# Kernel tuning notes

Measured on AMD Instinct MI355X. Metric: run time of the kernel, lower is better.

The kernel has to match this reference:

```python
import jax, jax.numpy as jnp
import numpy as np

B, L, H, NL = 32, 1024, 4, 2
D_BERT, D_PHY, D_ACC = 1024, 7, 2
C_IN = D_BERT + D_PHY + D_ACC
D = 32
K = 20
N = B * L
E = N * K


def setup_inputs() -> dict:
    key = jax.random.key(0)
    ks = jax.random.split(key, 10)
    return {
        "protbert": jax.random.normal(ks[0], (B, 1, L, D_BERT), jnp.float32),
        "phychem": jax.random.normal(ks[1], (B, 1, L, D_PHY), jnp.float32),
        "resacc": jax.random.normal(ks[2], (B, 1, L, D_ACC), jnp.float32),
        "edge_feat": jax.random.normal(ks[3], (E, 2), jnp.float32),
        "src_idx": jax.random.randint(ks[4], (E,), 0, N, jnp.int32),
        "dst_idx": (jnp.arange(E, dtype=jnp.int32) % N),  # every node gets exactly K in-edges
        "conv_w": jax.random.normal(ks[5], (D, C_IN, 7), jnp.float32) * 0.02,
        "conv_b": jnp.zeros((D,), jnp.float32),
        "bn_gamma": jnp.ones((D,), jnp.float32),
        "bn_beta": jnp.zeros((D,), jnp.float32),
        "bn_mean": jnp.zeros((D,), jnp.float32),
        "bn_var": jnp.ones((D,), jnp.float32),
        "fc_w": jax.random.normal(ks[6], (NL, H, D, D), jnp.float32) * 0.1,
        "attn_w": jax.random.normal(ks[7], (NL, H, 2 * D + 2), jnp.float32) * 0.1,
        "fc_edge_w": jax.random.normal(ks[8], (NL, H, D, 2), jnp.float32) * 0.1,
        "fc_eatt_w": jax.random.normal(ks[9], (NL, H, 2, 2), jnp.float32) * 0.1,
    }


def _leaky(x):
    return jnp.where(x >= 0, x, 0.01 * x)


def _seg_softmax(e, dst, n):
    # softmax over incoming edges of each destination node (DGL mailbox softmax)
    m = jax.ops.segment_max(e, dst, num_segments=n)
    ex = jnp.exp(e - m[dst])
    s = jax.ops.segment_sum(ex, dst, num_segments=n)
    return ex / s[dst]


def reference(protbert, phychem, resacc, edge_feat, src_idx, dst_idx,
              conv_w, conv_b, bn_gamma, bn_beta, bn_mean, bn_var,
              fc_w, attn_w, fc_edge_w, fc_eatt_w):
    # --- Conv1d + LeakyReLU + BatchNorm1d (eval) encoder ---
    x = jnp.concatenate([protbert, phychem, resacc], axis=3)[:, 0]  # (B,L,C_IN)
    x = jnp.transpose(x, (0, 2, 1))  # (B,C_IN,L)
    x = jax.lax.conv_general_dilated(x, conv_w, (1,), [(3, 3)],
                                     dimension_numbers=("NCH", "OIH", "NCH"))
    x = _leaky(x + conv_b[None, :, None])
    scale = (bn_gamma / jnp.sqrt(bn_var + 1e-5))[None, :, None]
    x = (x - bn_mean[None, :, None]) * scale + bn_beta[None, :, None]
    feats = jnp.transpose(x, (0, 2, 1))  # (B,L,D)

    # --- stacked multi-head EGRET layers on flattened batched graph ---
    h = feats.reshape(N, D)
    alpha = None
    for l in range(NL):
        z = jnp.einsum("nd,hod->nho", h, fc_w[l])                    # (N,H,D)
        ex_t = jnp.einsum("ef,hgf->ehg", edge_feat, fc_eatt_w[l])    # (E,H,2) transformed edge feats for attn
        ez = jnp.einsum("ef,hof->eho", edge_feat, fc_edge_w[l])      # (E,H,D) edge messages
        a_src = attn_w[l][:, :D]
        a_dst = attn_w[l][:, D:2 * D]
        a_e = attn_w[l][:, 2 * D:]
        s_src = jnp.einsum("nhd,hd->nh", z, a_src)                   # node-level partial scores
        s_dst = jnp.einsum("nhd,hd->nh", z, a_dst)
        e = _leaky(s_src[src_idx] + s_dst[dst_idx]
                   + jnp.einsum("ehg,hg->eh", ex_t, a_e))            # (E,H)
        alpha = _seg_softmax(e, dst_idx, N)                          # (E,H)
        msg = alpha[:, :, None] * (z[src_idx] + ez)                  # attn on node+edge messages
        h = jax.ops.segment_sum(msg, dst_idx, num_segments=N).mean(axis=1)  # merge='avg'

    feats2 = h.reshape(B, L, D)
    out = jnp.concatenate([feats2, feats], axis=2)  # (B,L,2D)
    return out, alpha
```

## Files before the change

kernel.cpp:

```cpp
#include <hip/hip_runtime.h>
#include <hip/hip_bf16.h>
#include <cstdint>

#define B_   32
#define L_   1024
#define H_   4
#define NL_  2
#define D_   32
#define K_   20
#define N_   (B_ * L_)
#define E_   (N_ * K_)

typedef __attribute__((ext_vector_type(8))) __bf16 bf16x8;
typedef __attribute__((ext_vector_type(4))) float  f32x4;
typedef __attribute__((ext_vector_type(2))) float  f32x2;
typedef __attribute__((ext_vector_type(4))) int    i32x4;

static __device__ __forceinline__ float leaky1(float x) { return x >= 0.f ? x : 0.01f * x; }

static __device__ __forceinline__ bf16x8 cvt8(f32x4 lo, f32x4 hi) {
    bf16x8 r;
    r[0] = (__bf16)lo[0]; r[1] = (__bf16)lo[1]; r[2] = (__bf16)lo[2]; r[3] = (__bf16)lo[3];
    r[4] = (__bf16)hi[0]; r[5] = (__bf16)hi[1]; r[6] = (__bf16)hi[2]; r[7] = (__bf16)hi[3];
    return r;
}

#define GLD_LDS16(g, l) __builtin_amdgcn_global_load_lds( \
    (const __attribute__((address_space(1))) void*)(g),   \
    (__attribute__((address_space(3))) void*)(l), 16, 0, 0)

__global__ __launch_bounds__(256) void k_prep_wb(const float* __restrict__ conv_w,
                                                 __bf16* __restrict__ wb) {
    int idx = blockIdx.x * 256 + threadIdx.x;
    if (idx >= 7 * 32 * 1024) return;
    int t = idx >> 15;
    int r = idx & 32767;
    int d = r >> 10;
    int c = r & 1023;
    wb[idx] = (__bf16)conv_w[d * 7231 + c * 7 + t];
}

#define XR4 262
__global__ __launch_bounds__(256) void k_conv_part(
    const float* __restrict__ protbert, const __bf16* __restrict__ wb,
    float* __restrict__ pbuf) {
    __shared__ __bf16 Xs[2][XR4 * 32];
    __shared__ __bf16 Bs[2][224 * 32];

    const int tid  = threadIdx.x;
    const int tok0 = blockIdx.x * 256;
    const int b    = tok0 >> 10;
    const int lb   = tok0 & 1023;
    const int cb0  = blockIdx.y * 256;

    const float* agp[5];
    int aoffv[5];
    bool ex[5];
    #pragma unroll
    for (int q = 0; q < 5; ++q) {
        int u = (q < 4) ? q * 256 + tid : 1024 + tid;
        bool e = (q < 4) || (tid < 24);
        int row = u >> 2, slot = u & 3;
        int l = lb + row - 3;
        ex[q] = e;
        aoffv[q] = row * 32 + 8 * (slot ^ ((row >> 1) & 3));
        agp[q] = (e && (unsigned)l < 1024u)
            ? protbert + ((size_t)b * 1024 + l) * 1024 + cb0 + slot * 8 : nullptr;
    }

    const int w     = tid >> 6;
    const int lane  = tid & 63;
    const int row16 = lane & 15;
    const int kgrp  = lane >> 4;
    const int d0    = lane & 15;
    const int bslot0 = 8 * (kgrp ^ ((d0 >> 1) & 3));

    const int blrow = lane >> 2;
    const int bsl   = lane & 3;
#define STAGE_B(kc_, bf_) do {                                              \
        for (int c = w; c < 14; c += 4) {                                   \
            int brow_ = c * 16 + blrow;                                     \
            int dd_ = brow_ & 31;                                           \
            int scol_ = 8 * (bsl ^ ((dd_ >> 1) & 3));                       \
            const __bf16* gp_ = wb + (size_t)brow_ * 1024 + cb0 + (kc_) * 32 + scol_; \
            GLD_LDS16(gp_, &Bs[bf_][c * 512]);                              \
        }                                                                   \
    } while (0)

    f32x4 acc[4][2];
    #pragma unroll
    for (int mt = 0; mt < 4; ++mt) {
        acc[mt][0] = (f32x4){0.f, 0.f, 0.f, 0.f};
        acc[mt][1] = (f32x4){0.f, 0.f, 0.f, 0.f};
    }

    {
        f32x4 pl[5], ph[5];
        #pragma unroll
        for (int q = 0; q < 5; ++q) {
            pl[q] = (f32x4){0,0,0,0}; ph[q] = (f32x4){0,0,0,0};
            if (agp[q]) { pl[q] = ((const f32x4*)agp[q])[0]; ph[q] = ((const f32x4*)agp[q])[1]; }
        }
        STAGE_B(0, 0);
        #pragma unroll
        for (int q = 0; q < 5; ++q)
            if (ex[q]) *(bf16x8*)(&Xs[0][aoffv[q]]) = cvt8(pl[q], ph[q]);
    }
    __syncthreads();

    int buf = 0;
    for (int kk = 0; kk < 8; ++kk) {
        f32x4 nl[5], nh[5];
        if (kk < 7) {
            #pragma unroll
            for (int q = 0; q < 5; ++q) {
                nl[q] = (f32x4){0,0,0,0}; nh[q] = (f32x4){0,0,0,0};
                if (agp[q]) {
                    nl[q] = ((const f32x4*)agp[q])[(kk + 1) * 8];
                    nh[q] = ((const f32x4*)agp[q])[(kk + 1) * 8 + 1];
                }
            }
            STAGE_B(kk + 1, buf ^ 1);
        }
        #pragma unroll
        for (int t = 0; t < 7; ++t) {
            bf16x8 b0 = *(const bf16x8*)(&Bs[buf][(t * 32 + d0) * 32 + bslot0]);
            bf16x8 b1 = *(const bf16x8*)(&Bs[buf][(t * 32 + 16 + d0) * 32 + bslot0]);
            #pragma unroll
            for (int mt = 0; mt < 4; ++mt) {
                int arow = w * 64 + mt * 16 + row16 + t;
                bf16x8 a = *(const bf16x8*)(&Xs[buf][arow * 32 + 8 * (kgrp ^ ((arow >> 1) & 3))]);
                acc[mt][0] = __builtin_amdgcn_mfma_f32_16x16x32_bf16(a, b0, acc[mt][0], 0, 0, 0);
                acc[mt][1] = __builtin_amdgcn_mfma_f32_16x16x32_bf16(a, b1, acc[mt][1], 0, 0, 0);
            }
        }
        if (kk < 7) {
            #pragma unroll
            for (int q = 0; q < 5; ++q)
                if (ex[q]) *(bf16x8*)(&Xs[buf ^ 1][aoffv[q]]) = cvt8(nl[q], nh[q]);
        }
        __syncthreads();
        buf ^= 1;
    }

    float* pb = pbuf + ((size_t)blockIdx.y * N_ + tok0) * 32;
    #pragma unroll
    for (int mt = 0; mt < 4; ++mt)
        #pragma unroll
        for (int i = 0; i < 4; ++i) {
            int lrow = w * 64 + mt * 16 + kgrp * 4 + i;
            pb[lrow * 32 + d0]      = acc[mt][0][i];
            pb[lrow * 32 + 16 + d0] = acc[mt][1][i];
        }
}

#define AROWS 70
__global__ __launch_bounds__(256) void k_epi_z0(
    const float* __restrict__ pbuf,     const float* __restrict__ phychem,
    const float* __restrict__ resacc,   const float* __restrict__ conv_w,
    const float* __restrict__ conv_b,   const float* __restrict__ bn_gamma,
    const float* __restrict__ bn_beta,  const float* __restrict__ bn_mean,
    const float* __restrict__ bn_var,   const float* __restrict__ fc_w,
    const float* __restrict__ attn_w,
    float* __restrict__ out, __bf16* __restrict__ z,
    float* __restrict__ ssrc, float* __restrict__ sdst) {
    __shared__ float WT[4 * 1028];
    __shared__ float As[4 * 33], Ad[4 * 33];
    __shared__ float x9[AROWS * 9];
    __shared__ float w9[9 * 7 * 32];
    __shared__ float bnA[32], bnB[32], cb[32];
    __shared__ float fs[64 * 36];

    const int tid  = threadIdx.x;
    const int tok0 = blockIdx.x * 64;
    const int b    = tok0 >> 10;
    const int lb   = tok0 & 1023;

    for (int i = tid; i < 4096; i += 256) {
        int h = i >> 10, rem = i & 1023, o = rem >> 5, d = rem & 31;
        WT[h * 1028 + d * 32 + o] = fc_w[i];
    }
    {
        int h = tid >> 6, o = tid & 63;
        float v = attn_w[h * 66 + o];
        if (o < 32) As[h * 33 + o] = v; else Ad[h * 33 + (o - 32)] = v;
    }
    for (int i = tid; i < 9 * 7 * 32; i += 256) {
        int d = i & 31, jt = i >> 5, t = jt % 7, j = jt / 7;
        w9[i] = conv_w[d * 7231 + (1024 + j) * 7 + t];
    }
    for (int i = tid; i < AROWS * 9; i += 256) {
        int r = i / 9, j = i % 9;
        int l = lb + r - 3;
        float v = 0.f;
        if ((unsigned)l < 1024u)
            v = (j < 7) ? phychem[(b * 1024 + l) * 7 + j] : resacc[(b * 1024 + l) * 2 + (j - 7)];
        x9[i] = v;
    }
    if (tid < 32) {
        float sc = bn_gamma[tid] * rsqrtf(bn_var[tid] + 1e-5f);
        bnA[tid] = sc;
        bnB[tid] = bn_beta[tid] - bn_mean[tid] * sc;
        cb[tid]  = conv_b[tid];
    }
    __syncthreads();

    {
        const int d  = tid & 31;
        const int r0 = tid >> 5;
        #pragma unroll
        for (int q = 0; q < 8; ++q) {
            int lrow = r0 * 8 + q;
            int tok  = tok0 + lrow;
            float s = pbuf[(size_t)tok * 32 + d]
                    + pbuf[(size_t)(N_ + tok) * 32 + d]
                    + pbuf[(size_t)(2 * N_ + tok) * 32 + d]
                    + pbuf[(size_t)(3 * N_ + tok) * 32 + d];
            float c = 0.f;
            #pragma unroll
            for (int t = 0; t < 7; ++t) {
                const float* xr = &x9[(lrow + t) * 9];
                #pragma unroll
                for (int j = 0; j < 9; ++j) c += xr[j] * w9[(j * 7 + t) * 32 + d];
            }
            float v = leaky1(s + c + cb[d]) * bnA[d] + bnB[d];
            out[(size_t)tok * 64 + 32 + d] = v;
            fs[lrow * 36 + d] = v;
        }
    }
    __syncthreads();

    {
        const int nl = tid >> 2;
        const int h  = tid & 3;
        const int n  = tok0 + nl;

        float hrow[32];
        const f32x4* h4 = (const f32x4*)(&fs[nl * 36]);
        #pragma unroll
        for (int q = 0; q < 8; ++q) {
            f32x4 v = h4[q];
            hrow[q * 4 + 0] = v[0]; hrow[q * 4 + 1] = v[1];
            hrow[q * 4 + 2] = v[2]; hrow[q * 4 + 3] = v[3];
        }
        float zz[32];
        #pragma unroll
        for (int o = 0; o < 32; ++o) zz[o] = 0.f;
        #pragma unroll
        for (int d = 0; d < 32; ++d) {
            float hv = hrow[d];
            const f32x4* wt = (const f32x4*)&WT[h * 1028 + d * 32];
            #pragma unroll
            for (int o4 = 0; o4 < 8; ++o4) {
                f32x4 wv = wt[o4];
                zz[o4 * 4 + 0] += hv * wv[0]; zz[o4 * 4 + 1] += hv * wv[1];
                zz[o4 * 4 + 2] += hv * wv[2]; zz[o4 * 4 + 3] += hv * wv[3];
            }
        }
        float s1 = 0.f, s2 = 0.f;
        #pragma unroll
        for (int o = 0; o < 32; ++o) {
            s1 += zz[o] * As[h * 33 + o];
            s2 += zz[o] * Ad[h * 33 + o];
        }
        bf16x8* zo = (bf16x8*)(z + (size_t)n * 128 + h * 32);
        #pragma unroll
        for (int q = 0; q < 4; ++q) {
            bf16x8 v;
            #pragma unroll
            for (int j = 0; j < 8; ++j) v[j] = (__bf16)zz[q * 8 + j];
            zo[q] = v;
        }
        ssrc[n * 4 + h] = s1;
        sdst[n * 4 + h] = s2;
    }
}

__global__ __launch_bounds__(256) void k_z(
    const float* __restrict__ hin, const float* __restrict__ fc_w,
    const float* __restrict__ attn_w, int layer,
    __bf16* __restrict__ z, float* __restrict__ ssrc, float* __restrict__ sdst) {
    __shared__ float WT[4 * 1028];
    __shared__ float As[4 * 33], Ad[4 * 33];

    const int tid = threadIdx.x;
    for (int i = tid; i < 4096; i += 256) {
        int h = i >> 10, rem = i & 1023, o = rem >> 5, d = rem & 31;
        WT[h * 1028 + d * 32 + o] = fc_w[layer * 4096 + i];
    }
    {
        int h = tid >> 6, o = tid & 63;
        float v = attn_w[layer * (4 * 66) + h * 66 + o];
        if (o < 32) As[h * 33 + o] = v; else Ad[h * 33 + (o - 32)] = v;
    }
    __syncthreads();

    const int n = blockIdx.x * 64 + (tid >> 2);
    const int h = tid & 3;

    float hrow[32];
    const f32x4* h4 = (const f32x4*)(hin + (size_t)n * 32);
    #pragma unroll
    for (int q = 0; q < 8; ++q) {
        f32x4 v = h4[q];
        hrow[q * 4 + 0] = v[0]; hrow[q * 4 + 1] = v[1];
        hrow[q * 4 + 2] = v[2]; hrow[q * 4 + 3] = v[3];
    }

    float zz[32];
    #pragma unroll
    for (int o = 0; o < 32; ++o) zz[o] = 0.f;
    #pragma unroll
    for (int d = 0; d < 32; ++d) {
        float hv = hrow[d];
        const f32x4* wt = (const f32x4*)&WT[h * 1028 + d * 32];
        #pragma unroll
        for (int o4 = 0; o4 < 8; ++o4) {
            f32x4 wv = wt[o4];
            zz[o4 * 4 + 0] += hv * wv[0]; zz[o4 * 4 + 1] += hv * wv[1];
            zz[o4 * 4 + 2] += hv * wv[2]; zz[o4 * 4 + 3] += hv * wv[3];
        }
    }
    float s1 = 0.f, s2 = 0.f;
    #pragma unroll
    for (int o = 0; o < 32; ++o) {
        s1 += zz[o] * As[h * 33 + o];
        s2 += zz[o] * Ad[h * 33 + o];
    }
    bf16x8* zo = (bf16x8*)(z + (size_t)n * 128 + h * 32);
    #pragma unroll
    for (int q = 0; q < 4; ++q) {
        bf16x8 v;
        #pragma unroll
        for (int j = 0; j < 8; ++j) v[j] = (__bf16)zz[q * 8 + j];
        zo[q] = v;
    }
    ssrc[n * 4 + h] = s1;
    sdst[n * 4 + h] = s2;
}

__global__ __launch_bounds__(256) void k_node(
    const __bf16* __restrict__ z, const float* __restrict__ ssrc,
    const float* __restrict__ sdst, const int* __restrict__ src_idx,
    const float* __restrict__ edge_feat, const float* __restrict__ attn_w,
    const float* __restrict__ fc_edge_w, const float* __restrict__ fc_eatt_w,
    int layer, float* __restrict__ hout, int hout_stride,
    float* __restrict__ alpha_out) {
    __shared__ float sWe0[4 * 32], sWe1[4 * 32];
    __shared__ float sP[4][2];
    __shared__ float sAl[4][4][24];
    __shared__ float sF[4][4][2];
    __shared__ float sEf[4][20][2];
    __shared__ int   sS[4][24];

    const int tid = threadIdx.x;
    {
        int f = tid & 1, dd = (tid >> 1) & 31, h = tid >> 6;
        float v = fc_edge_w[layer * 256 + tid];
        if (f == 0) sWe0[h * 32 + dd] = v; else sWe1[h * 32 + dd] = v;
        if (tid < 8) {
            int hh = tid >> 1, ff = tid & 1;
            float ae0 = attn_w[layer * 264 + hh * 66 + 64];
            float ae1 = attn_w[layer * 264 + hh * 66 + 65];
            float w0  = fc_eatt_w[layer * 16 + hh * 4 + 0 + ff];
            float w1  = fc_eatt_w[layer * 16 + hh * 4 + 2 + ff];
            sP[hh][ff] = ae0 * w0 + ae1 * w1;
        }
    }
    const int slot = tid >> 6, tn = tid & 63;
    const int n = blockIdx.x * 4 + slot;
    __syncthreads();

    {
        int h = tn & 3;
        float sdv = sdst[n * 4 + h];
        #pragma unroll
        for (int p = 0; p < 2; ++p) {
            int k = p * 16 + (tn >> 2);
            if (p == 0 || tn < 16) {
                int e = n + k * N_;
                int s = src_idx[e];
                f32x2 ef = *(const f32x2*)(edge_feat + (size_t)e * 2);
                float sc = ssrc[s * 4 + h] + sdv + ef.x * sP[h][0] + ef.y * sP[h][1];
                sAl[slot][h][k] = leaky1(sc);
                if (h == 0) { sS[slot][k] = s; sEf[slot][k][0] = ef.x; sEf[slot][k][1] = ef.y; }
            }
        }
    }
    __syncthreads();

    if (tn < 4) {
        int h = tn;
        float m = -1e30f;
        for (int k = 0; k < 20; ++k) m = fmaxf(m, sAl[slot][h][k]);
        float ssum = 0.f;
        for (int k = 0; k < 20; ++k) {
            float v = __expf(sAl[slot][h][k] - m);
            sAl[slot][h][k] = v;
            ssum += v;
        }
        float inv = 1.f / ssum;
        float F0 = 0.f, F1 = 0.f;
        for (int k = 0; k < 20; ++k) {
            float a = sAl[slot][h][k] * inv;
            sAl[slot][h][k] = a;
            F0 += a * sEf[slot][k][0];
            F1 += a * sEf[slot][k][1];
        }
        sF[slot][h][0] = F0;
        sF[slot][h][1] = F1;
    }
    __syncthreads();

    if (alpha_out != nullptr) {
        #pragma unroll
        for (int p = 0; p < 2; ++p) {
            int k = p * 16 + (tn >> 2), h = tn & 3;
            if (p == 0 || tn < 16)
                alpha_out[(size_t)(n + k * N_) * 4 + h] = sAl[slot][h][k];
        }
    }

    {
        const int h = tn >> 4, dp = tn & 15;
        f32x4 areg[5];
        i32x4 sreg[5];
        #pragma unroll
        for (int q = 0; q < 5; ++q) {
            areg[q] = *(const f32x4*)(&sAl[slot][h][q * 4]);
            sreg[q] = *(const i32x4*)(&sS[slot][q * 4]);
        }
        float F0 = sF[slot][h][0], F1 = sF[slot][h][1];
        float w0a = sWe0[h * 32 + dp * 2], w0b = sWe0[h * 32 + dp * 2 + 1];
        float w1a = sWe1[h * 32 + dp * 2], w1b = sWe1[h * 32 + dp * 2 + 1];
        float acca = F0 * w0a + F1 * w1a;
        float accb = F0 * w0b + F1 * w1b;
        #pragma unroll
        for (int k = 0; k < 20; ++k) {
            int sk = __builtin_amdgcn_readfirstlane(sreg[k >> 2][k & 3]);
            const uint32_t* zp = (const uint32_t*)(z + (size_t)sk * 128);
            uint32_t u = zp[tn];
            float zl = __uint_as_float(u << 16);
            float zh = __uint_as_float(u & 0xffff0000u);
            float a = areg[k >> 2][k & 3];
            acca = fmaf(a, zl, acca);
            accb = fmaf(a, zh, accb);
        }
        acca += __shfl_xor(acca, 16); acca += __shfl_xor(acca, 32);
        accb += __shfl_xor(accb, 16); accb += __shfl_xor(accb, 32);
        if (tn < 16) {
            f32x2 o = {0.25f * acca, 0.25f * accb};
            *(f32x2*)(hout + (size_t)n * hout_stride + dp * 2) = o;
        }
    }
}

extern "C" void kernel_launch(void* const* d_in, const int* in_sizes, int n_in,
                              void* d_out, int out_size, void* d_ws, size_t ws_size,
                              hipStream_t stream) {
    const float* protbert  = (const float*)d_in[0];
    const float* phychem   = (const float*)d_in[1];
    const float* resacc    = (const float*)d_in[2];
    const float* edge_feat = (const float*)d_in[3];
    const int*   src_idx   = (const int*)d_in[4];
    const float* conv_w    = (const float*)d_in[6];
    const float* conv_b    = (const float*)d_in[7];
    const float* bn_gamma  = (const float*)d_in[8];
    const float* bn_beta   = (const float*)d_in[9];
    const float* bn_mean   = (const float*)d_in[10];
    const float* bn_var    = (const float*)d_in[11];
    const float* fc_w      = (const float*)d_in[12];
    const float* attn_w    = (const float*)d_in[13];
    const float* fc_edge_w = (const float*)d_in[14];
    const float* fc_eatt_w = (const float*)d_in[15];

    char* ws = (char*)d_ws;
    __bf16* wb   = (__bf16*)(ws);
    float* h1    = (float*)(ws + (5u  << 20));
    float* ssrc  = (float*)(ws + (9u  << 20));
    float* sdst  = (float*)(ws + (10u << 20));
    __bf16* z    = (__bf16*)(ws + (11u << 20));
    float* pbuf  = (float*)(ws + (24u << 20));

    float* out       = (float*)d_out;
    float* alpha_out = out + (size_t)N_ * 64;

    k_prep_wb<<<896, 256, 0, stream>>>(conv_w, wb);
    k_conv_part<<<dim3(128, 4), 256, 0, stream>>>(protbert, wb, pbuf);
    k_epi_z0<<<512, 256, 0, stream>>>(pbuf, phychem, resacc, conv_w, conv_b,
                                      bn_gamma, bn_beta, bn_mean, bn_var,
                                      fc_w, attn_w, out, z, ssrc, sdst);
    k_node<<<N_ / 4, 256, 0, stream>>>(z, ssrc, sdst, src_idx, edge_feat, attn_w,
                                       fc_edge_w, fc_eatt_w, 0, h1, 32, nullptr);
    k_z<<<512, 256, 0, stream>>>(h1, fc_w, attn_w, 1, z, ssrc, sdst);
    k_node<<<N_ / 4, 256, 0, stream>>>(z, ssrc, sdst, src_idx, edge_feat, attn_w,
                                       fc_edge_w, fc_eatt_w, 1, out, 64, alpha_out);
}
```

Measured before the change: 136.2 us.

## Fuse layer-1 projection into first node kernel and store conv partials in bf16

The second layer's node projection (z = h·W, plus the src/dst attention scores) now runs inside the first k_node launch. That kernel writes z2/ssrc2/sdst2 directly, so the h1 round trip and the separate k_z launch are gone. Separate ping-pong buffers for z and the scores avoid races between blocks. The conv partial-sum buffer is also stored as bf16 instead of fp32, which halves its traffic at some cost in accuracy. Each k_node block now loads a 4096-float weight tile into shared memory, which adds LDS use and may reduce occupancy.

```diff
diff --git a/kernel.cpp b/kernel.cpp
--- a/kernel.cpp
+++ b/kernel.cpp
@@ -43,7 +43,7 @@
 #define XR4 262
 __global__ __launch_bounds__(256) void k_conv_part(
     const float* __restrict__ protbert, const __bf16* __restrict__ wb,
-    float* __restrict__ pbuf) {
+    __bf16* __restrict__ pbuf) {
     __shared__ __bf16 Xs[2][XR4 * 32];
     __shared__ __bf16 Bs[2][224 * 32];
 
@@ -143,20 +143,20 @@
         buf ^= 1;
     }
 
-    float* pb = pbuf + ((size_t)blockIdx.y * N_ + tok0) * 32;
+    __bf16* pb = pbuf + ((size_t)blockIdx.y * N_ + tok0) * 32;
     #pragma unroll
     for (int mt = 0; mt < 4; ++mt)
         #pragma unroll
         for (int i = 0; i < 4; ++i) {
             int lrow = w * 64 + mt * 16 + kgrp * 4 + i;
-            pb[lrow * 32 + d0]      = acc[mt][0][i];
-            pb[lrow * 32 + 16 + d0] = acc[mt][1][i];
+            pb[lrow * 32 + d0]      = (__bf16)acc[mt][0][i];
+            pb[lrow * 32 + 16 + d0] = (__bf16)acc[mt][1][i];
         }
 }
 
 #define AROWS 70
 __global__ __launch_bounds__(256) void k_epi_z0(
-    const float* __restrict__ pbuf,     const float* __restrict__ phychem,
+    const __bf16* __restrict__ pbuf,    const float* __restrict__ phychem,
     const float* __restrict__ resacc,   const float* __restrict__ conv_w,
     const float* __restrict__ conv_b,   const float* __restrict__ bn_gamma,
     const float* __restrict__ bn_beta,  const float* __restrict__ bn_mean,
@@ -212,10 +212,10 @@
         for (int q = 0; q < 8; ++q) {
             int lrow = r0 * 8 + q;
             int tok  = tok0 + lrow;
-            float s = pbuf[(size_t)tok * 32 + d]
-                    + pbuf[(size_t)(N_ + tok) * 32 + d]
-                    + pbuf[(size_t)(2 * N_ + tok) * 32 + d]
-                    + pbuf[(size_t)(3 * N_ + tok) * 32 + d];
+            float s = (float)pbuf[(size_t)tok * 32 + d]
+                    + (float)pbuf[(size_t)(N_ + tok) * 32 + d]
+                    + (float)pbuf[(size_t)(2 * N_ + tok) * 32 + d]
+                    + (float)pbuf[(size_t)(3 * N_ + tok) * 32 + d];
             float c = 0.f;
             #pragma unroll
             for (int t = 0; t < 7; ++t) {
@@ -274,69 +274,6 @@
         ssrc[n * 4 + h] = s1;
         sdst[n * 4 + h] = s2;
     }
-}
-
-__global__ __launch_bounds__(256) void k_z(
-    const float* __restrict__ hin, const float* __restrict__ fc_w,
-    const float* __restrict__ attn_w, int layer,
-    __bf16* __restrict__ z, float* __restrict__ ssrc, float* __restrict__ sdst) {
-    __shared__ float WT[4 * 1028];
-    __shared__ float As[4 * 33], Ad[4 * 33];
-
-    const int tid = threadIdx.x;
-    for (int i = tid; i < 4096; i += 256) {
-        int h = i >> 10, rem = i & 1023, o = rem >> 5, d = rem & 31;
-        WT[h * 1028 + d * 32 + o] = fc_w[layer * 4096 + i];
-    }
-    {
-        int h = tid >> 6, o = tid & 63;
-        float v = attn_w[layer * (4 * 66) + h * 66 + o];
-        if (o < 32) As[h * 33 + o] = v; else Ad[h * 33 + (o - 32)] = v;
-    }
-    __syncthreads();
-
-    const int n = blockIdx.x * 64 + (tid >> 2);
-    const int h = tid & 3;
-
-    float hrow[32];
-    const f32x4* h4 = (const f32x4*)(hin + (size_t)n * 32);
-    #pragma unroll
-    for (int q = 0; q < 8; ++q) {
-        f32x4 v = h4[q];
-        hrow[q * 4 + 0] = v[0]; hrow[q * 4 + 1] = v[1];
-        hrow[q * 4 + 2] = v[2]; hrow[q * 4 + 3] = v[3];
-    }
-
-    float zz[32];
-    #pragma unroll
-    for (int o = 0; o < 32; ++o) zz[o] = 0.f;
-    #pragma unroll
-    for (int d = 0; d < 32; ++d) {
-        float hv = hrow[d];
-        const f32x4* wt = (const f32x4*)&WT[h * 1028 + d * 32];
-        #pragma unroll
-        for (int o4 = 0; o4 < 8; ++o4) {
-            f32x4 wv = wt[o4];
-            zz[o4 * 4 + 0] += hv * wv[0]; zz[o4 * 4 + 1] += hv * wv[1];
-            zz[o4 * 4 + 2] += hv * wv[2]; zz[o4 * 4 + 3] += hv * wv[3];
-        }
-    }
-    float s1 = 0.f, s2 = 0.f;
-    #pragma unroll
-    for (int o = 0; o < 32; ++o) {
-        s1 += zz[o] * As[h * 33 + o];
-        s2 += zz[o] * Ad[h * 33 + o];
-    }
-    bf16x8* zo = (bf16x8*)(z + (size_t)n * 128 + h * 32);
-    #pragma unroll
-    for (int q = 0; q < 4; ++q) {
-        bf16x8 v;
-        #pragma unroll
-        for (int j = 0; j < 8; ++j) v[j] = (__bf16)zz[q * 8 + j];
-        zo[q] = v;
-    }
-    ssrc[n * 4 + h] = s1;
-    sdst[n * 4 + h] = s2;
 }
 
 __global__ __launch_bounds__(256) void k_node(
@@ -345,13 +282,18 @@
     const float* __restrict__ edge_feat, const float* __restrict__ attn_w,
     const float* __restrict__ fc_edge_w, const float* __restrict__ fc_eatt_w,
     int layer, float* __restrict__ hout, int hout_stride,
-    float* __restrict__ alpha_out) {
+    float* __restrict__ alpha_out, const float* __restrict__ fc_w,
+    __bf16* __restrict__ zout, float* __restrict__ ssrc_out,
+    float* __restrict__ sdst_out) {
     __shared__ float sWe0[4 * 32], sWe1[4 * 32];
     __shared__ float sP[4][2];
     __shared__ float sAl[4][4][24];
     __shared__ float sF[4][4][2];
     __shared__ float sEf[4][20][2];
     __shared__ int   sS[4][24];
+    __shared__ float sW1[128 * 33];
+    __shared__ float As1[4 * 33], Ad1[4 * 33];
+    __shared__ float sH[4][32];
 
     const int tid = threadIdx.x;
     {
@@ -367,6 +309,17 @@
             sP[hh][ff] = ae0 * w0 + ae1 * w1;
         }
     }
+    if (zout != nullptr) {
+        for (int i = tid; i < 4096; i += 256) {
+            int h = i >> 10, o = (i >> 5) & 31, d = i & 31;
+            sW1[(h * 32 + o) * 33 + d] = fc_w[4096 + i];
+        }
+        {
+            int h = tid >> 6, o = tid & 63;
+            float v = attn_w[264 + h * 66 + o];
+            if (o < 32) As1[h * 33 + o] = v; else Ad1[h * 33 + (o - 32)] = v;
+        }
+    }
     const int slot = tid >> 6, tn = tid & 63;
     const int n = blockIdx.x * 4 + slot;
     __syncthreads();
@@ -448,9 +401,44 @@
         }
         acca += __shfl_xor(acca, 16); acca += __shfl_xor(acca, 32);
         accb += __shfl_xor(accb, 16); accb += __shfl_xor(accb, 32);
-        if (tn < 16) {
-            f32x2 o = {0.25f * acca, 0.25f * accb};
-            *(f32x2*)(hout + (size_t)n * hout_stride + dp * 2) = o;
+        if (zout == nullptr) {
+            if (tn < 16) {
+                f32x2 o = {0.25f * acca, 0.25f * accb};
+                *(f32x2*)(hout + (size_t)n * hout_stride + dp * 2) = o;
+            }
+        } else {
+            if (tn < 16) {
+                sH[slot][dp * 2]     = 0.25f * acca;
+                sH[slot][dp * 2 + 1] = 0.25f * accb;
+            }
+        }
+    }
+
+    if (zout != nullptr) {
+        __syncthreads();
+        const int h = tn >> 4, og = tn & 15;
+        const float* hr = sH[slot];
+        const float* w0r = &sW1[(h * 32 + og * 2) * 33];
+        const float* w1r = &sW1[(h * 32 + og * 2 + 1) * 33];
+        float z0v = 0.f, z1v = 0.f;
+        #pragma unroll
+        for (int d = 0; d < 32; ++d) {
+            float hv = hr[d];
+            z0v = fmaf(hv, w0r[d], z0v);
+            z1v = fmaf(hv, w1r[d], z1v);
+        }
+        __bf16* zp = zout + (size_t)n * 128 + h * 32 + og * 2;
+        zp[0] = (__bf16)z0v;
+        zp[1] = (__bf16)z1v;
+        float ps = z0v * As1[h * 33 + og * 2] + z1v * As1[h * 33 + og * 2 + 1];
+        float pd = z0v * Ad1[h * 33 + og * 2] + z1v * Ad1[h * 33 + og * 2 + 1];
+        ps += __shfl_xor(ps, 1); ps += __shfl_xor(ps, 2);
+        ps += __shfl_xor(ps, 4); ps += __shfl_xor(ps, 8);
+        pd += __shfl_xor(pd, 1); pd += __shfl_xor(pd, 2);
+        pd += __shfl_xor(pd, 4); pd += __shfl_xor(pd, 8);
+        if (og == 0) {
+            ssrc_out[n * 4 + h] = ps;
+            sdst_out[n * 4 + h] = pd;
         }
     }
 }
@@ -475,12 +463,14 @@
     const float* fc_eatt_w = (const float*)d_in[15];
 
     char* ws = (char*)d_ws;
-    __bf16* wb   = (__bf16*)(ws);
-    float* h1    = (float*)(ws + (5u  << 20));
-    float* ssrc  = (float*)(ws + (9u  << 20));
-    float* sdst  = (float*)(ws + (10u << 20));
-    __bf16* z    = (__bf16*)(ws + (11u << 20));
-    float* pbuf  = (float*)(ws + (24u << 20));
+    __bf16* wb    = (__bf16*)(ws);
+    float* ssrc   = (float*)(ws + (9u  << 20));
+    float* sdst   = (float*)(ws + (10u << 20));
+    __bf16* z     = (__bf16*)(ws + (11u << 20));
+    float* ssrc2  = (float*)(ws + (20u << 20));
+    float* sdst2  = (float*)(ws + (21u << 20));
+    __bf16* pbuf  = (__bf16*)(ws + (24u << 20));
+    __bf16* z2    = (__bf16*)(ws + (33u << 20));
 
     float* out       = (float*)d_out;
     float* alpha_out = out + (size_t)N_ * 64;
@@ -491,8 +481,9 @@
                                       bn_gamma, bn_beta, bn_mean, bn_var,
                                       fc_w, attn_w, out, z, ssrc, sdst);
     k_node<<<N_ / 4, 256, 0, stream>>>(z, ssrc, sdst, src_idx, edge_feat, attn_w,
-                                       fc_edge_w, fc_eatt_w, 0, h1, 32, nullptr);
-    k_z<<<512, 256, 0, stream>>>(h1, fc_w, attn_w, 1, z, ssrc, sdst);
-    k_node<<<N_ / 4, 256, 0, stream>>>(z, ssrc, sdst, src_idx, edge_feat, attn_w,
-                                       fc_edge_w, fc_eatt_w, 1, out, 64, alpha_out);
-}
+                                       fc_edge_w, fc_eatt_w, 0, nullptr, 0, nullptr,
+                                       fc_w, z2, ssrc2, sdst2);
+    k_node<<<N_ / 4, 256, 0, stream>>>(z2, ssrc2, sdst2, src_idx, edge_feat, attn_w,
+                                       fc_edge_w, fc_eatt_w, 1, out, 64, alpha_out,
+                                       fc_w, nullptr, nullptr, nullptr);
+}
```

After: 139.5 us. +2.5%, slower.
